# Performance work log

Hardware: AMD Instinct MI355X
Metric: run time of the kernel (lower is better)

## Reference

```python
import jax, jax.numpy as jnp
import numpy as np

N, E, IN, OUT, R, B = 20000, 640000, 128, 128, 65, 65
BN_EPS = 1e-5


def setup_inputs() -> dict:
    key = jax.random.key(0)
    ks = jax.random.split(key, 8)
    node_feats = jax.random.normal(ks[0], (N, IN), dtype=jnp.float32)
    src = jax.random.randint(ks[1], (E,), 0, N, dtype=jnp.int32)
    dst = jax.random.randint(ks[2], (E,), 0, N, dtype=jnp.int32)
    etype = jax.random.randint(ks[3], (E,), 0, R, dtype=jnp.int32)
    norm = jax.random.uniform(ks[4], (E, 1), dtype=jnp.float32)
    basis = jax.random.normal(ks[5], (B, IN, OUT), dtype=jnp.float32) * 0.05
    comp = jax.random.normal(ks[6], (R, B), dtype=jnp.float32) * 0.1
    h_bias = jnp.zeros((OUT,), dtype=jnp.float32)
    W_res = jax.random.normal(ks[7], (IN, OUT), dtype=jnp.float32) * 0.05
    b_res = jnp.zeros((OUT,), dtype=jnp.float32)
    gamma = jnp.ones((OUT,), dtype=jnp.float32)
    beta = jnp.zeros((OUT,), dtype=jnp.float32)
    return dict(node_feats=node_feats, src=src, dst=dst, etype=etype, norm=norm,
                basis=basis, comp=comp, h_bias=h_bias, W_res=W_res, b_res=b_res,
                gamma=gamma, beta=beta)


def reference(node_feats, src, dst, etype, norm, basis, comp, h_bias, W_res, b_res, gamma, beta):
    n, in_f = node_feats.shape
    r = comp.shape[0]
    # Basis decomposition: W_r = sum_b comp[r,b] * basis[b]  -> (R, in, out)
    W = jnp.einsum('rb,bio->rio', comp, basis)
    # Per-edge message x[src] * norm (norm is scalar per edge so it commutes
    # with the relation matmul). Aggregate per (dst, relation) first, then do
    # one dense relation-batched GEMM (mathematically identical to DGL's
    # per-edge transform + scatter-add, since everything is linear).
    msg = node_feats[src] * norm                       # (E, in)
    seg = dst.astype(jnp.int32) * r + etype            # combined (dst, rel) key
    S = jax.ops.segment_sum(msg, seg, num_segments=n * r).reshape(n, r, in_f)
    h = jnp.einsum('nri,rio->no', S, W) + h_bias       # (N, out)
    h = jax.nn.relu(h)                                 # conv activation (dropout p=0)
    # Residual branch: relu(Linear(x))
    h = h + jax.nn.relu(node_feats @ W_res + b_res)
    # BatchNorm1d (training mode: batch stats, biased variance)
    mean = jnp.mean(h, axis=0)
    var = jnp.var(h, axis=0)
    h = (h - mean) * jax.lax.rsqrt(var + BN_EPS) * gamma + beta
    return h
```

## Files before the change

### kernel.cpp

```cpp
#include <hip/hip_runtime.h>
#include <hip/hip_bf16.h>


#define N_NODES 20000
#define E_EDGES 640000
#define R_REL   65
#define TM      128
#define NB_RESID 313
#define MAX_TILES 5120
#define SCAT_CH 2560

typedef __attribute__((ext_vector_type(8))) short bf16x8;
typedef __attribute__((ext_vector_type(4))) float f32x4;
typedef __attribute__((ext_vector_type(4))) unsigned int u32x4;
typedef __attribute__((ext_vector_type(2))) unsigned int u32x2;

__device__ __forceinline__ unsigned short f2bf(float x) {
    union { float f; unsigned int u; } c; c.f = x;
    unsigned int b = c.u + 0x7fffu + ((c.u >> 16) & 1u);
    return (unsigned short)(b >> 16);
}
__device__ __forceinline__ float bf2f_lo(unsigned int u) {
    union { unsigned int u; float f; } c; c.u = u << 16; return c.f;
}
__device__ __forceinline__ float bf2f_hi(unsigned int u) {
    union { unsigned int u; float f; } c; c.u = u & 0xffff0000u; return c.f;
}
__device__ __forceinline__ void async16(const void* g, void* l) {
    __builtin_amdgcn_global_load_lds(
        (const __attribute__((address_space(1))) unsigned int*)g,
        (__attribute__((address_space(3))) unsigned int*)l, 16, 0, 0);
}
__device__ __forceinline__ int unperm(int p) {
    return (p & 64) + ((p & 3) << 4) + ((p >> 2) & 15);
}

__global__ void k_prep1(const float* __restrict__ comp, const float* __restrict__ basis,
                        float* __restrict__ W32, const int* __restrict__ et,
                        const int* __restrict__ dstA, int* __restrict__ ghist,
                        int* __restrict__ gh2, const float* __restrict__ node_feats,
                        unsigned short* __restrict__ node_bf) {
    __shared__ float lc[16 * 65];
    __shared__ int lh[R_REL];
    int b = blockIdx.x, t = threadIdx.x;
    if (b < 320) {
        int r0 = (b >> 6) * 16;
        int col = (b & 63) * 256 + t;
        for (int j = t; j < 16 * 65; j += 256) {
            int rr = r0 + j / 65;
            lc[j] = (rr < R_REL) ? comp[rr * 65 + (j % 65)] : 0.f;
        }
        __syncthreads();
        float acc[16];
#pragma unroll
        for (int j = 0; j < 16; ++j) acc[j] = 0.f;
        for (int k = 0; k < 65; ++k) {
            float v = basis[k * 16384 + col];
#pragma unroll
            for (int j = 0; j < 16; ++j) acc[j] += lc[j * 65 + k] * v;
        }
#pragma unroll
        for (int j = 0; j < 16; ++j) {
            int rr = r0 + j;
            if (rr < R_REL) W32[rr * 16384 + col] = acc[j];
        }
    } else if (b < 832) {
        if (t < R_REL) lh[t] = 0;
        __syncthreads();
        for (int i = (b - 320) * 256 + t; i < E_EDGES; i += 512 * 256) {
            atomicAdd(&lh[et[i]], 1);
            atomicAdd(&gh2[dstA[i]], 1);
        }
        __syncthreads();
        if (t < R_REL) atomicAdd(&ghist[t], lh[t]);
    } else {
        int i = (b - 832) * 256 + t;
        if (i < N_NODES * 32) {
            float4 v = reinterpret_cast<const float4*>(node_feats)[i];
            __hip_bfloat162 b0 = __float22bfloat162_rn(make_float2(v.x, v.y));
            __hip_bfloat162 b1 = __float22bfloat162_rn(make_float2(v.z, v.w));
            u32x2 pk;
            pk.x = *reinterpret_cast<unsigned int*>(&b0);
            pk.y = *reinterpret_cast<unsigned int*>(&b1);
            reinterpret_cast<u32x2*>(node_bf)[i] = pk;
        }
    }
}

__global__ void k_prep3(const int* __restrict__ gh2, int* __restrict__ cnt2,
                        int* __restrict__ seg, const int* __restrict__ ghist,
                        int* __restrict__ cnt, int* __restrict__ ntiles_p,
                        int* __restrict__ tile_rel, int* __restrict__ tile_start,
                        int* __restrict__ tile_len, const float* __restrict__ W32,
                        unsigned short* __restrict__ Wt, const float* __restrict__ Wresf,
                        unsigned short* __restrict__ Wrest) {
    int b = blockIdx.x, t = threadIdx.x;
    if (b < 80) {
        __shared__ int red[256];
        __shared__ int pref;
        int acc = 0;
        for (int i = t; i < b * 256; i += 256) acc += gh2[i];
        red[t] = acc;
        __syncthreads();
        for (int off = 128; off > 0; off >>= 1) {
            if (t < off) red[t] += red[t + off];
            __syncthreads();
        }
        if (t == 0) pref = red[0];
        __syncthreads();
        int i = b * 256 + t;
        int v = (i < N_NODES) ? gh2[i] : 0;
        red[t] = v;
        __syncthreads();
        for (int off = 1; off < 256; off <<= 1) {
            int x = (t >= off) ? red[t - off] : 0;
            __syncthreads();
            red[t] += x;
            __syncthreads();
        }
        int excl = red[t] - v + pref;
        if (i < N_NODES) {
            cnt2[i] = excl;
            seg[i] = excl;
            if (i == N_NODES - 1) seg[N_NODES] = excl + v;
        }
    } else if (b == 80) {
        __shared__ int base[R_REL + 1], tbase[R_REL + 1];
        int lane = t & 63;
        if (t < 64) {
            int v = ghist[lane];
            int x = v;
#pragma unroll
            for (int off = 1; off < 64; off <<= 1) {
                int y = __shfl_up(x, off);
                if (lane >= off) x += y;
            }
            base[lane] = x - v;
            if (lane == 63) {
                base[64] = x;
                base[65] = x + ghist[64];
            }
        }
        __syncthreads();
        if (t == 0) {
            int tb = 0;
            for (int r = 0; r < R_REL; ++r) {
                tbase[r] = tb;
                tb += (base[r + 1] - base[r] + TM - 1) / TM;
            }
            *ntiles_p = tb;
        }
        __syncthreads();
        if (t < R_REL) {
            cnt[t] = base[t];
            int s = base[t], e = base[t + 1], j = tbase[t];
            while (s < e) {
                int len = min(TM, e - s);
                tile_rel[j] = t; tile_start[j] = s; tile_len[j] = len;
                ++j; s += len;
            }
        }
    } else {
        __shared__ float tile[64][65];
        int bb = b - 81;
        const float* s; unsigned short* d; int sub;
        if (bb < R_REL * 4) { s = W32 + (size_t)(bb >> 2) * 16384; d = Wt + (size_t)(bb >> 2) * 16384; sub = bb & 3; }
        else { s = Wresf; d = Wrest; sub = bb - R_REL * 4; }
        int ot = (sub >> 1) & 1, itl = sub & 1;
        int tx = t & 63, ty = t >> 6;
        for (int it = 0; it < 16; ++it) {
            int i = ty + it * 4;
            tile[i][tx] = s[(itl * 64 + i) * 128 + ot * 64 + tx];
        }
        __syncthreads();
        for (int it = 0; it < 16; ++it) {
            int o = ty + it * 4;
            d[(ot * 64 + o) * 128 + itl * 64 + tx] = f2bf(tile[tx][o]);
        }
    }
}

__global__ void k_scatter2(const int* __restrict__ et, const int* __restrict__ srcA,
                           const int* __restrict__ dstA, const float* __restrict__ norm,
                           int* __restrict__ cnt, int* __restrict__ cnt2,
                           int* __restrict__ srcp, float* __restrict__ normp,
                           int* __restrict__ eidx) {
    __shared__ int lh[R_REL], lbase[R_REL];
    int c0 = blockIdx.x * SCAT_CH;
    int cend = min(c0 + SCAT_CH, E_EDGES);
    if (threadIdx.x < R_REL) lh[threadIdx.x] = 0;
    __syncthreads();
    for (int i = c0 + threadIdx.x; i < cend; i += 256) atomicAdd(&lh[et[i]], 1);
    __syncthreads();
    if (threadIdx.x < R_REL && lh[threadIdx.x] > 0)
        lbase[threadIdx.x] = atomicAdd(&cnt[threadIdx.x], lh[threadIdx.x]);
    __syncthreads();
    if (threadIdx.x < R_REL) lh[threadIdx.x] = 0;
    __syncthreads();
    for (int i = c0 + threadIdx.x; i < cend; i += 256) {
        int r = et[i];
        int p = lbase[r] + atomicAdd(&lh[r], 1);
        srcp[p] = srcA[i];
        normp[p] = norm[i];
        int pos = atomicAdd(&cnt2[dstA[i]], 1);
        eidx[pos] = p;
    }
}

__global__ __launch_bounds__(256, 2) void k_conv_gemm(
    const int* __restrict__ tile_rel, const int* __restrict__ tile_start,
    const int* __restrict__ tile_len, const int* __restrict__ ntiles_p,
    const int* __restrict__ srcp, const float* __restrict__ normp,
    const unsigned short* __restrict__ node_bf,
    const unsigned short* __restrict__ Wt, const unsigned short* __restrict__ Wrest,
    const float* __restrict__ b_res, unsigned short* __restrict__ t_out,
    float* __restrict__ resid) {
    __shared__ unsigned short Alds[128 * 128];
    __shared__ unsigned short Blds[128 * 128];
    __shared__ float snorm[128];
    int t = threadIdx.x;
    int w = t >> 6, lane = t & 63;
    int lrow = lane & 15, quad = lane >> 4;

    if (blockIdx.x < NB_RESID) {
        int wr = (w >> 1) * 32, wc = (w & 1) * 64;
        int row0 = blockIdx.x * 64;
        int nrows = min(64, N_NODES - row0);
#pragma unroll
        for (int it = 0; it < 8; ++it) {
            int j = t + 256 * it;
            int o = j >> 4, c = j & 15, cs = c ^ (o & 15);
            async16(Wrest + o * 128 + cs * 8, &Blds[o * 128 + c * 8]);
        }
#pragma unroll
        for (int it = 0; it < 4; ++it) {
            int j = t + 256 * it;
            int p = j >> 4, c = j & 15, cs = c ^ (p & 15);
            if (p < nrows)
                async16(node_bf + (size_t)(row0 + p) * 128 + cs * 8,
                        &Alds[p * 128 + c * 8]);
        }
        __syncthreads();
        f32x4 acc[2][4];
#pragma unroll
        for (int i = 0; i < 2; ++i)
#pragma unroll
            for (int j = 0; j < 4; ++j) acc[i][j] = (f32x4){0.f, 0.f, 0.f, 0.f};
#pragma unroll
        for (int ks = 0; ks < 4; ++ks) {
            int cs = (ks * 4 + quad) ^ lrow;
            bf16x8 af[2], bfr[4];
#pragma unroll
            for (int i = 0; i < 2; ++i)
                af[i] = *reinterpret_cast<const bf16x8*>(&Alds[(wr + i * 16 + lrow) * 128 + cs * 8]);
#pragma unroll
            for (int j = 0; j < 4; ++j)
                bfr[j] = *reinterpret_cast<const bf16x8*>(&Blds[(wc + j * 16 + lrow) * 128 + cs * 8]);
#pragma unroll
            for (int i = 0; i < 2; ++i)
#pragma unroll
                for (int j = 0; j < 4; ++j)
                    acc[i][j] = __builtin_amdgcn_mfma_f32_16x16x32_bf16(af[i], bfr[j], acc[i][j], 0, 0, 0);
        }
        float br0 = b_res[wc + lrow];
        float br1 = b_res[wc + 16 + lrow];
        float br2 = b_res[wc + 32 + lrow];
        float br3 = b_res[wc + 48 + lrow];
#pragma unroll
        for (int i = 0; i < 2; ++i) {
#pragma unroll
            for (int reg = 0; reg < 4; ++reg) {
                int grow = row0 + wr + i * 16 + quad * 4 + reg;
                if (grow < N_NODES) {
                    float4 v;
                    v.x = fmaxf(acc[i][0][reg] + br0, 0.f);
                    v.y = fmaxf(acc[i][1][reg] + br1, 0.f);
                    v.z = fmaxf(acc[i][2][reg] + br2, 0.f);
                    v.w = fmaxf(acc[i][3][reg] + br3, 0.f);
                    *reinterpret_cast<float4*>(resid + (size_t)grow * 128 + wc + lrow * 4) = v;
                }
            }
        }
        return;
    }

    int tid = blockIdx.x - NB_RESID;
    if (tid >= *ntiles_p) return;
    int r = tile_rel[tid], start = tile_start[tid], len = tile_len[tid];
    int wr = w * 32;
    const unsigned short* Wr = Wt + (size_t)r * 16384;
#pragma unroll
    for (int it = 0; it < 8; ++it) {
        int j = t + 256 * it;
        int o = j >> 4, c = j & 15, cs = c ^ (o & 15);
        async16(Wr + o * 128 + cs * 8, &Blds[o * 128 + c * 8]);
    }
#pragma unroll
    for (int it = 0; it < 8; ++it) {
        int j = t + 256 * it;
        int p = j >> 4, c = j & 15, cs = c ^ (p & 15);
        if (p < len)
            async16(node_bf + (size_t)srcp[start + p] * 128 + cs * 8,
                    &Alds[p * 128 + c * 8]);
    }
    if (t < TM && t < len) snorm[t] = normp[start + t];
    __syncthreads();

    f32x4 acc[2][8];
#pragma unroll
    for (int i = 0; i < 2; ++i)
#pragma unroll
        for (int j = 0; j < 8; ++j) acc[i][j] = (f32x4){0.f, 0.f, 0.f, 0.f};
#pragma unroll
    for (int ks = 0; ks < 4; ++ks) {
        int cs = (ks * 4 + quad) ^ lrow;
        bf16x8 af[2], bfr[8];
#pragma unroll
        for (int i = 0; i < 2; ++i)
            af[i] = *reinterpret_cast<const bf16x8*>(&Alds[(wr + i * 16 + lrow) * 128 + cs * 8]);
#pragma unroll
        for (int j = 0; j < 8; ++j)
            bfr[j] = *reinterpret_cast<const bf16x8*>(&Blds[(j * 16 + lrow) * 128 + cs * 8]);
#pragma unroll
        for (int i = 0; i < 2; ++i)
#pragma unroll
            for (int j = 0; j < 8; ++j)
                acc[i][j] = __builtin_amdgcn_mfma_f32_16x16x32_bf16(af[i], bfr[j], acc[i][j], 0, 0, 0);
    }

#pragma unroll
    for (int i = 0; i < 2; ++i) {
        int m0 = wr + i * 16 + quad * 4;
#pragma unroll
        for (int reg = 0; reg < 4; ++reg) {
            int m = m0 + reg;
            if (m < len) {
                float nm = snorm[m];
                float2 l0 = make_float2(acc[i][0][reg] * nm, acc[i][1][reg] * nm);
                float2 l1 = make_float2(acc[i][2][reg] * nm, acc[i][3][reg] * nm);
                float2 h0 = make_float2(acc[i][4][reg] * nm, acc[i][5][reg] * nm);
                float2 h1 = make_float2(acc[i][6][reg] * nm, acc[i][7][reg] * nm);
                __hip_bfloat162 bl0 = __float22bfloat162_rn(l0);
                __hip_bfloat162 bl1 = __float22bfloat162_rn(l1);
                __hip_bfloat162 bh0 = __float22bfloat162_rn(h0);
                __hip_bfloat162 bh1 = __float22bfloat162_rn(h1);
                u32x2 s0, s1;
                s0.x = *reinterpret_cast<unsigned int*>(&bl0);
                s0.y = *reinterpret_cast<unsigned int*>(&bl1);
                s1.x = *reinterpret_cast<unsigned int*>(&bh0);
                s1.y = *reinterpret_cast<unsigned int*>(&bh1);
                unsigned short* rowp = t_out + (size_t)(start + m) * 128;
                *reinterpret_cast<u32x2*>(rowp + lrow * 4)      = s0;
                *reinterpret_cast<u32x2*>(rowp + 64 + lrow * 4) = s1;
            }
        }
    }
}

__global__ __launch_bounds__(256) void k_reduce_fused(
    const unsigned short* __restrict__ t, const int* __restrict__ seg,
    const int* __restrict__ eidx, const float* __restrict__ resid,
    const float* __restrict__ h_bias, float* __restrict__ h,
    float* __restrict__ colsum, float* __restrict__ colsumsq) {
    __shared__ float cs1[128], cs2[128], sbias[128];
    if (threadIdx.x < 128) {
        cs1[threadIdx.x] = 0.f; cs2[threadIdx.x] = 0.f;
        sbias[threadIdx.x] = h_bias[unperm(threadIdx.x)];
    }
    __syncthreads();
    int w = threadIdx.x >> 6, lane = threadIdx.x & 63;
    int g = lane >> 4, c = lane & 15;
    for (int k = 0; k < 2; ++k) {
        int d = blockIdx.x * 8 + k * 4 + w;
        int a = seg[d], b = seg[d + 1];
        float s[8];
#pragma unroll
        for (int kk = 0; kk < 8; ++kk) s[kk] = 0.f;
        for (int q = a + g; q < b; q += 32) {
            int er[8];
#pragma unroll
            for (int kk = 0; kk < 8; ++kk) {
                int row = q + 4 * kk;
                er[kk] = eidx[(row < b) ? row : a];
            }
            u32x4 v[8];
#pragma unroll
            for (int kk = 0; kk < 8; ++kk) {
                v[kk] = *reinterpret_cast<const u32x4*>(t + (size_t)er[kk] * 128 + c * 8);
                if (q + 4 * kk >= b) v[kk] = (u32x4){0u, 0u, 0u, 0u};
            }
#pragma unroll
            for (int kk = 0; kk < 8; ++kk)
#pragma unroll
                for (int j = 0; j < 4; ++j) {
                    s[2 * j]     += bf2f_lo(v[kk][j]);
                    s[2 * j + 1] += bf2f_hi(v[kk][j]);
                }
        }
#pragma unroll
        for (int kk = 0; kk < 8; ++kk) {
            s[kk] += __shfl_xor(s[kk], 16);
            s[kk] += __shfl_xor(s[kk], 32);
        }
        if (g == 0) {
            const float* rp = resid + (size_t)d * 128 + c * 8;
            float4 r0 = *reinterpret_cast<const float4*>(rp);
            float4 r1 = *reinterpret_cast<const float4*>(rp + 4);
            float rr[8] = {r0.x, r0.y, r0.z, r0.w, r1.x, r1.y, r1.z, r1.w};
            float v[8];
#pragma unroll
            for (int kk = 0; kk < 8; ++kk)
                v[kk] = fmaxf(s[kk] + sbias[c * 8 + kk], 0.f) + rr[kk];
            float* hp = h + (size_t)d * 128 + c * 8;
            *reinterpret_cast<float4*>(hp)     = make_float4(v[0], v[1], v[2], v[3]);
            *reinterpret_cast<float4*>(hp + 4) = make_float4(v[4], v[5], v[6], v[7]);
#pragma unroll
            for (int kk = 0; kk < 8; ++kk) {
                atomicAdd(&cs1[c * 8 + kk], v[kk]);
                atomicAdd(&cs2[c * 8 + kk], v[kk] * v[kk]);
            }
        }
    }
    __syncthreads();
    if (threadIdx.x < 128) {
        atomicAdd(&colsum[threadIdx.x], cs1[threadIdx.x]);
        atomicAdd(&colsumsq[threadIdx.x], cs2[threadIdx.x]);
    }
}

__global__ void k_bn(float* __restrict__ h, const float* __restrict__ colsum,
                     const float* __restrict__ colsumsq, const float* __restrict__ gamma,
                     const float* __restrict__ beta) {
    __shared__ float sc[128], sh[128], tile[8][128];
    int t = threadIdx.x;
    if (t < 128) {
        int n = unperm(t);
        float m = colsum[t] * (1.f / N_NODES);
        float var = colsumsq[t] * (1.f / N_NODES) - m * m;
        float s = gamma[n] * rsqrtf(var + 1e-5f);
        sc[t] = s;
        sh[t] = beta[n] - m * s;
    }
    __syncthreads();
    int r = t >> 5;
    int p0 = (t & 31) * 4;
    int n0 = (p0 & 64) + ((p0 >> 2) & 15);
    for (int row0 = blockIdx.x * 8; row0 < N_NODES; row0 += gridDim.x * 8) {
        int row = row0 + r;
        float4 v = make_float4(0.f, 0.f, 0.f, 0.f);
        if (row < N_NODES) v = *reinterpret_cast<float4*>(h + (size_t)row * 128 + p0);
        v.x = v.x * sc[p0] + sh[p0];
        v.y = v.y * sc[p0 + 1] + sh[p0 + 1];
        v.z = v.z * sc[p0 + 2] + sh[p0 + 2];
        v.w = v.w * sc[p0 + 3] + sh[p0 + 3];
        tile[r][n0]      = v.x;
        tile[r][n0 + 16] = v.y;
        tile[r][n0 + 32] = v.z;
        tile[r][n0 + 48] = v.w;
        __syncthreads();
        if (row < N_NODES)
            *reinterpret_cast<float4*>(h + (size_t)row * 128 + p0) =
                *reinterpret_cast<float4*>(&tile[r][p0]);
        __syncthreads();
    }
}

extern "C" void kernel_launch(void* const* d_in, const int* in_sizes, int n_in,
                              void* d_out, int out_size, void* d_ws, size_t ws_size,
                              hipStream_t stream) {
    (void)in_sizes; (void)n_in; (void)out_size; (void)ws_size;
    const float* node_feats = (const float*)d_in[0];
    const int* src    = (const int*)d_in[1];
    const int* dst    = (const int*)d_in[2];
    const int* etype  = (const int*)d_in[3];
    const float* norm = (const float*)d_in[4];
    const float* basis = (const float*)d_in[5];
    const float* comp  = (const float*)d_in[6];
    const float* h_bias = (const float*)d_in[7];
    const float* W_res  = (const float*)d_in[8];
    const float* b_res  = (const float*)d_in[9];
    const float* gamma  = (const float*)d_in[10];
    const float* beta   = (const float*)d_in[11];

    char* ws = (char*)d_ws;
    int* ghist      = (int*)(ws + 0);
    int* cnt        = (int*)(ws + 1024);
    int* ntiles_p   = (int*)(ws + 2048);
    float* colsum   = (float*)(ws + 2560);
    float* colsumsq = (float*)(ws + 3072);
    int* gh2        = (int*)(ws + 8192);
    int* tile_rel   = (int*)(ws + 88192);
    int* tile_start = (int*)(ws + 129152);
    int* tile_len   = (int*)(ws + 170112);
    unsigned short* Wt      = (unsigned short*)(ws + 211072);
    unsigned short* Wrest   = (unsigned short*)(ws + 2340992);
    unsigned short* node_bf = (unsigned short*)(ws + 2373760);
    int* srcp       = (int*)(ws + 7493760);
    float* normp    = (float*)(ws + 10053760);
    int* eidx       = (int*)(ws + 12613760);
    float* resid    = (float*)(ws + 15173760);
    int* seg        = (int*)(ws + 25413760);
    int* cnt2       = (int*)(ws + 25493776);
    const long T_BASE = 25573776L;
    float* W32      = (float*)(ws + T_BASE);
    unsigned short* t_buf = (unsigned short*)(ws + T_BASE);
    float* hacc = (float*)d_out;

    hipMemsetAsync(ws, 0, 88192, stream);
    k_prep1<<<3332, 256, 0, stream>>>(comp, basis, W32, etype, dst, ghist, gh2,
                                      node_feats, node_bf);
    k_prep3<<<345, 256, 0, stream>>>(gh2, cnt2, seg, ghist, cnt, ntiles_p,
                                     tile_rel, tile_start, tile_len,
                                     W32, Wt, W_res, Wrest);
    k_scatter2<<<(E_EDGES + SCAT_CH - 1) / SCAT_CH, 256, 0, stream>>>(
        etype, src, dst, norm, cnt, cnt2, srcp, normp, eidx);
    k_conv_gemm<<<NB_RESID + MAX_TILES, 256, 0, stream>>>(
        tile_rel, tile_start, tile_len, ntiles_p, srcp, normp, node_bf,
        Wt, Wrest, b_res, t_buf, resid);
    k_reduce_fused<<<N_NODES / 8, 256, 0, stream>>>(t_buf, seg, eidx, resid,
                                                    h_bias, hacc, colsum, colsumsq);
    k_bn<<<2500, 256, 0, stream>>>(hacc, colsum, colsumsq, gamma, beta);
}
```

Baseline: 344.5 us.

## Bucket edges by (dst group, relation) so transformed rows gather locally

Edges are now sorted by a combined key of destination group (dst>>7) and relation instead of by relation alone, using a per-key histogram, scan and direct atomic scatter. Tiles are built per key with a smaller TM of 64, and the GEMM kernel uses a 64-row A tile with launch bounds raised to allow more blocks per CU. The intent is that the per-edge transformed rows read by the reduce kernel sit close together in memory, improving cache locality of the gather, and that occupancy rises. The cost is many more, smaller, partially filled tiles, each of which reloads a full 128x128 weight block. Edge order inside a bucket now depends on atomic ordering, and the reduce kernel processes 32 nodes per block.

```diff
diff --git a/kernel.cpp b/kernel.cpp
--- a/kernel.cpp
+++ b/kernel.cpp
@@ -5,10 +5,11 @@
 #define N_NODES 20000
 #define E_EDGES 640000
 #define R_REL   65
-#define TM      128
+#define NGRP_B  157
+#define NKEY_B  (NGRP_B * R_REL)
 #define NB_RESID 313
-#define MAX_TILES 5120
-#define SCAT_CH 2560
+#define MAX_TILES 20480
+#define TM      64
 
 typedef __attribute__((ext_vector_type(8))) short bf16x8;
 typedef __attribute__((ext_vector_type(4))) float f32x4;
@@ -37,11 +38,10 @@
 
 __global__ void k_prep1(const float* __restrict__ comp, const float* __restrict__ basis,
                         float* __restrict__ W32, const int* __restrict__ et,
-                        const int* __restrict__ dstA, int* __restrict__ ghist,
+                        const int* __restrict__ dstA, int* __restrict__ gh3,
                         int* __restrict__ gh2, const float* __restrict__ node_feats,
                         unsigned short* __restrict__ node_bf) {
     __shared__ float lc[16 * 65];
-    __shared__ int lh[R_REL];
     int b = blockIdx.x, t = threadIdx.x;
     if (b < 320) {
         int r0 = (b >> 6) * 16;
@@ -65,14 +65,11 @@
             if (rr < R_REL) W32[rr * 16384 + col] = acc[j];
         }
     } else if (b < 832) {
-        if (t < R_REL) lh[t] = 0;
-        __syncthreads();
         for (int i = (b - 320) * 256 + t; i < E_EDGES; i += 512 * 256) {
-            atomicAdd(&lh[et[i]], 1);
-            atomicAdd(&gh2[dstA[i]], 1);
-        }
-        __syncthreads();
-        if (t < R_REL) atomicAdd(&ghist[t], lh[t]);
+            int d = dstA[i];
+            atomicAdd(&gh3[(d >> 7) * 65 + et[i]], 1);
+            atomicAdd(&gh2[d], 1);
+        }
     } else {
         int i = (b - 832) * 256 + t;
         if (i < N_NODES * 32) {
@@ -87,19 +84,17 @@
     }
 }
 
-__global__ void k_prep3(const int* __restrict__ gh2, int* __restrict__ cnt2,
-                        int* __restrict__ seg, const int* __restrict__ ghist,
-                        int* __restrict__ cnt, int* __restrict__ ntiles_p,
-                        int* __restrict__ tile_rel, int* __restrict__ tile_start,
-                        int* __restrict__ tile_len, const float* __restrict__ W32,
-                        unsigned short* __restrict__ Wt, const float* __restrict__ Wresf,
-                        unsigned short* __restrict__ Wrest) {
+__global__ void k_prep3(const int* __restrict__ gh3, int* __restrict__ segB,
+                        int* __restrict__ cnt3, const int* __restrict__ gh2,
+                        int* __restrict__ cnt2, int* __restrict__ seg,
+                        const float* __restrict__ W32, unsigned short* __restrict__ Wt,
+                        const float* __restrict__ Wresf, unsigned short* __restrict__ Wrest) {
     int b = blockIdx.x, t = threadIdx.x;
-    if (b < 80) {
+    if (b < 40) {
         __shared__ int red[256];
         __shared__ int pref;
         int acc = 0;
-        for (int i = t; i < b * 256; i += 256) acc += gh2[i];
+        for (int i = t; i < b * 256; i += 256) acc += gh3[i];
         red[t] = acc;
         __syncthreads();
         for (int off = 128; off > 0; off >>= 1) {
@@ -109,7 +104,7 @@
         if (t == 0) pref = red[0];
         __syncthreads();
         int i = b * 256 + t;
-        int v = (i < N_NODES) ? gh2[i] : 0;
+        int v = (i < NKEY_B) ? gh3[i] : 0;
         red[t] = v;
         __syncthreads();
         for (int off = 1; off < 256; off <<= 1) {
@@ -119,50 +114,44 @@
             __syncthreads();
         }
         int excl = red[t] - v + pref;
+        if (i < NKEY_B) {
+            segB[i] = excl;
+            cnt3[i] = excl;
+            if (i == NKEY_B - 1) segB[NKEY_B] = excl + v;
+        }
+    } else if (b < 120) {
+        __shared__ int red[256];
+        __shared__ int pref;
+        int b2 = b - 40;
+        int acc = 0;
+        for (int i = t; i < b2 * 256; i += 256) acc += gh2[i];
+        red[t] = acc;
+        __syncthreads();
+        for (int off = 128; off > 0; off >>= 1) {
+            if (t < off) red[t] += red[t + off];
+            __syncthreads();
+        }
+        if (t == 0) pref = red[0];
+        __syncthreads();
+        int i = b2 * 256 + t;
+        int v = (i < N_NODES) ? gh2[i] : 0;
+        red[t] = v;
+        __syncthreads();
+        for (int off = 1; off < 256; off <<= 1) {
+            int x = (t >= off) ? red[t - off] : 0;
+            __syncthreads();
+            red[t] += x;
+            __syncthreads();
+        }
+        int excl = red[t] - v + pref;
         if (i < N_NODES) {
             cnt2[i] = excl;
             seg[i] = excl;
             if (i == N_NODES - 1) seg[N_NODES] = excl + v;
         }
-    } else if (b == 80) {
-        __shared__ int base[R_REL + 1], tbase[R_REL + 1];
-        int lane = t & 63;
-        if (t < 64) {
-            int v = ghist[lane];
-            int x = v;
-#pragma unroll
-            for (int off = 1; off < 64; off <<= 1) {
-                int y = __shfl_up(x, off);
-                if (lane >= off) x += y;
-            }
-            base[lane] = x - v;
-            if (lane == 63) {
-                base[64] = x;
-                base[65] = x + ghist[64];
-            }
-        }
-        __syncthreads();
-        if (t == 0) {
-            int tb = 0;
-            for (int r = 0; r < R_REL; ++r) {
-                tbase[r] = tb;
-                tb += (base[r + 1] - base[r] + TM - 1) / TM;
-            }
-            *ntiles_p = tb;
-        }
-        __syncthreads();
-        if (t < R_REL) {
-            cnt[t] = base[t];
-            int s = base[t], e = base[t + 1], j = tbase[t];
-            while (s < e) {
-                int len = min(TM, e - s);
-                tile_rel[j] = t; tile_start[j] = s; tile_len[j] = len;
-                ++j; s += len;
-            }
-        }
     } else {
         __shared__ float tile[64][65];
-        int bb = b - 81;
+        int bb = b - 120;
         const float* s; unsigned short* d; int sub;
         if (bb < R_REL * 4) { s = W32 + (size_t)(bb >> 2) * 16384; d = Wt + (size_t)(bb >> 2) * 16384; sub = bb & 3; }
         else { s = Wresf; d = Wrest; sub = bb - R_REL * 4; }
@@ -182,42 +171,51 @@
 
 __global__ void k_scatter2(const int* __restrict__ et, const int* __restrict__ srcA,
                            const int* __restrict__ dstA, const float* __restrict__ norm,
-                           int* __restrict__ cnt, int* __restrict__ cnt2,
+                           int* __restrict__ cnt3, int* __restrict__ cnt2,
                            int* __restrict__ srcp, float* __restrict__ normp,
-                           int* __restrict__ eidx) {
-    __shared__ int lh[R_REL], lbase[R_REL];
-    int c0 = blockIdx.x * SCAT_CH;
-    int cend = min(c0 + SCAT_CH, E_EDGES);
-    if (threadIdx.x < R_REL) lh[threadIdx.x] = 0;
-    __syncthreads();
-    for (int i = c0 + threadIdx.x; i < cend; i += 256) atomicAdd(&lh[et[i]], 1);
-    __syncthreads();
-    if (threadIdx.x < R_REL && lh[threadIdx.x] > 0)
-        lbase[threadIdx.x] = atomicAdd(&cnt[threadIdx.x], lh[threadIdx.x]);
-    __syncthreads();
-    if (threadIdx.x < R_REL) lh[threadIdx.x] = 0;
-    __syncthreads();
-    for (int i = c0 + threadIdx.x; i < cend; i += 256) {
-        int r = et[i];
-        int p = lbase[r] + atomicAdd(&lh[r], 1);
+                           int* __restrict__ eidx, const int* __restrict__ segB,
+                           int* __restrict__ ntiles_p, int* __restrict__ tile_r,
+                           int* __restrict__ tile_start, int* __restrict__ tile_len) {
+    int b = blockIdx.x, t = threadIdx.x;
+    if (b < 2500) {
+        int i = b * 256 + t;
+        if (i >= E_EDGES) return;
+        int d = dstA[i];
+        int key = (d >> 7) * 65 + et[i];
+        int p = atomicAdd(&cnt3[key], 1);
         srcp[p] = srcA[i];
         normp[p] = norm[i];
-        int pos = atomicAdd(&cnt2[dstA[i]], 1);
+        int pos = atomicAdd(&cnt2[d], 1);
         eidx[pos] = p;
-    }
-}
-
-__global__ __launch_bounds__(256, 2) void k_conv_gemm(
-    const int* __restrict__ tile_rel, const int* __restrict__ tile_start,
+    } else {
+        int i = (b - 2500) * 256 + t;
+        if (i < NKEY_B) {
+            int s = segB[i], e = segB[i + 1];
+            int len = e - s;
+            if (len > 0) {
+                int nt = (len + TM - 1) / TM;
+                int base = atomicAdd(ntiles_p, nt);
+                for (int k = 0; k < nt; ++k) {
+                    tile_r[base + k] = i % 65;
+                    tile_start[base + k] = s + k * TM;
+                    tile_len[base + k] = min(TM, len - k * TM);
+                }
+            }
+        }
+    }
+}
+
+__global__ __launch_bounds__(256, 3) void k_conv_gemm(
+    const int* __restrict__ tile_r, const int* __restrict__ tile_start,
     const int* __restrict__ tile_len, const int* __restrict__ ntiles_p,
     const int* __restrict__ srcp, const float* __restrict__ normp,
     const unsigned short* __restrict__ node_bf,
     const unsigned short* __restrict__ Wt, const unsigned short* __restrict__ Wrest,
     const float* __restrict__ b_res, unsigned short* __restrict__ t_out,
     float* __restrict__ resid) {
-    __shared__ unsigned short Alds[128 * 128];
     __shared__ unsigned short Blds[128 * 128];
-    __shared__ float snorm[128];
+    __shared__ unsigned short Alds[64 * 128];
+    __shared__ float snorm[64];
     int t = threadIdx.x;
     int w = t >> 6, lane = t & 63;
     int lrow = lane & 15, quad = lane >> 4;
@@ -286,8 +284,7 @@
 
     int tid = blockIdx.x - NB_RESID;
     if (tid >= *ntiles_p) return;
-    int r = tile_rel[tid], start = tile_start[tid], len = tile_len[tid];
-    int wr = w * 32;
+    int r = tile_r[tid], start = tile_start[tid], len = tile_len[tid];
     const unsigned short* Wr = Wt + (size_t)r * 16384;
 #pragma unroll
     for (int it = 0; it < 8; ++it) {
@@ -296,7 +293,7 @@
         async16(Wr + o * 128 + cs * 8, &Blds[o * 128 + c * 8]);
     }
 #pragma unroll
-    for (int it = 0; it < 8; ++it) {
+    for (int it = 0; it < 4; ++it) {
         int j = t + 256 * it;
         int p = j >> 4, c = j & 15, cs = c ^ (p & 15);
         if (p < len)
@@ -306,53 +303,43 @@
     if (t < TM && t < len) snorm[t] = normp[start + t];
     __syncthreads();
 
-    f32x4 acc[2][8];
-#pragma unroll
-    for (int i = 0; i < 2; ++i)
-#pragma unroll
-        for (int j = 0; j < 8; ++j) acc[i][j] = (f32x4){0.f, 0.f, 0.f, 0.f};
+    int wr = w * 16;
+    if (wr >= len) return;
+    f32x4 acc[8];
+#pragma unroll
+    for (int j = 0; j < 8; ++j) acc[j] = (f32x4){0.f, 0.f, 0.f, 0.f};
 #pragma unroll
     for (int ks = 0; ks < 4; ++ks) {
         int cs = (ks * 4 + quad) ^ lrow;
-        bf16x8 af[2], bfr[8];
-#pragma unroll
-        for (int i = 0; i < 2; ++i)
-            af[i] = *reinterpret_cast<const bf16x8*>(&Alds[(wr + i * 16 + lrow) * 128 + cs * 8]);
-#pragma unroll
-        for (int j = 0; j < 8; ++j)
-            bfr[j] = *reinterpret_cast<const bf16x8*>(&Blds[(j * 16 + lrow) * 128 + cs * 8]);
-#pragma unroll
-        for (int i = 0; i < 2; ++i)
-#pragma unroll
-            for (int j = 0; j < 8; ++j)
-                acc[i][j] = __builtin_amdgcn_mfma_f32_16x16x32_bf16(af[i], bfr[j], acc[i][j], 0, 0, 0);
-    }
-
-#pragma unroll
-    for (int i = 0; i < 2; ++i) {
-        int m0 = wr + i * 16 + quad * 4;
-#pragma unroll
-        for (int reg = 0; reg < 4; ++reg) {
-            int m = m0 + reg;
-            if (m < len) {
-                float nm = snorm[m];
-                float2 l0 = make_float2(acc[i][0][reg] * nm, acc[i][1][reg] * nm);
-                float2 l1 = make_float2(acc[i][2][reg] * nm, acc[i][3][reg] * nm);
-                float2 h0 = make_float2(acc[i][4][reg] * nm, acc[i][5][reg] * nm);
-                float2 h1 = make_float2(acc[i][6][reg] * nm, acc[i][7][reg] * nm);
-                __hip_bfloat162 bl0 = __float22bfloat162_rn(l0);
-                __hip_bfloat162 bl1 = __float22bfloat162_rn(l1);
-                __hip_bfloat162 bh0 = __float22bfloat162_rn(h0);
-                __hip_bfloat162 bh1 = __float22bfloat162_rn(h1);
-                u32x2 s0, s1;
-                s0.x = *reinterpret_cast<unsigned int*>(&bl0);
-                s0.y = *reinterpret_cast<unsigned int*>(&bl1);
-                s1.x = *reinterpret_cast<unsigned int*>(&bh0);
-                s1.y = *reinterpret_cast<unsigned int*>(&bh1);
-                unsigned short* rowp = t_out + (size_t)(start + m) * 128;
-                *reinterpret_cast<u32x2*>(rowp + lrow * 4)      = s0;
-                *reinterpret_cast<u32x2*>(rowp + 64 + lrow * 4) = s1;
-            }
+        bf16x8 af = *reinterpret_cast<const bf16x8*>(&Alds[(wr + lrow) * 128 + cs * 8]);
+#pragma unroll
+        for (int j = 0; j < 8; ++j) {
+            bf16x8 bfr = *reinterpret_cast<const bf16x8*>(&Blds[(j * 16 + lrow) * 128 + cs * 8]);
+            acc[j] = __builtin_amdgcn_mfma_f32_16x16x32_bf16(af, bfr, acc[j], 0, 0, 0);
+        }
+    }
+
+#pragma unroll
+    for (int reg = 0; reg < 4; ++reg) {
+        int m = wr + quad * 4 + reg;
+        if (m < len) {
+            float nm = snorm[m];
+            float2 l0 = make_float2(acc[0][reg] * nm, acc[1][reg] * nm);
+            float2 l1 = make_float2(acc[2][reg] * nm, acc[3][reg] * nm);
+            float2 h0 = make_float2(acc[4][reg] * nm, acc[5][reg] * nm);
+            float2 h1 = make_float2(acc[6][reg] * nm, acc[7][reg] * nm);
+            __hip_bfloat162 bl0 = __float22bfloat162_rn(l0);
+            __hip_bfloat162 bl1 = __float22bfloat162_rn(l1);
+            __hip_bfloat162 bh0 = __float22bfloat162_rn(h0);
+            __hip_bfloat162 bh1 = __float22bfloat162_rn(h1);
+            u32x2 s0, s1;
+            s0.x = *reinterpret_cast<unsigned int*>(&bl0);
+            s0.y = *reinterpret_cast<unsigned int*>(&bl1);
+            s1.x = *reinterpret_cast<unsigned int*>(&bh0);
+            s1.y = *reinterpret_cast<unsigned int*>(&bh1);
+            unsigned short* rowp = t_out + (size_t)(start + m) * 128;
+            *reinterpret_cast<u32x2*>(rowp + lrow * 4)      = s0;
+            *reinterpret_cast<u32x2*>(rowp + 64 + lrow * 4) = s1;
         }
     }
 }
@@ -370,8 +357,9 @@
     __syncthreads();
     int w = threadIdx.x >> 6, lane = threadIdx.x & 63;
     int g = lane >> 4, c = lane & 15;
-    for (int k = 0; k < 2; ++k) {
-        int d = blockIdx.x * 8 + k * 4 + w;
+    for (int k = 0; k < 8; ++k) {
+        int d = blockIdx.x * 32 + k * 4 + w;
+        if (d >= N_NODES) continue;
         int a = seg[d], b = seg[d + 1];
         float s[8];
 #pragma unroll
@@ -483,41 +471,42 @@
     const float* beta   = (const float*)d_in[11];
 
     char* ws = (char*)d_ws;
-    int* ghist      = (int*)(ws + 0);
-    int* cnt        = (int*)(ws + 1024);
-    int* ntiles_p   = (int*)(ws + 2048);
-    float* colsum   = (float*)(ws + 2560);
-    float* colsumsq = (float*)(ws + 3072);
-    int* gh2        = (int*)(ws + 8192);
-    int* tile_rel   = (int*)(ws + 88192);
-    int* tile_start = (int*)(ws + 129152);
-    int* tile_len   = (int*)(ws + 170112);
-    unsigned short* Wt      = (unsigned short*)(ws + 211072);
-    unsigned short* Wrest   = (unsigned short*)(ws + 2340992);
-    unsigned short* node_bf = (unsigned short*)(ws + 2373760);
-    int* srcp       = (int*)(ws + 7493760);
-    float* normp    = (float*)(ws + 10053760);
-    int* eidx       = (int*)(ws + 12613760);
-    float* resid    = (float*)(ws + 15173760);
-    int* seg        = (int*)(ws + 25413760);
-    int* cnt2       = (int*)(ws + 25493776);
-    const long T_BASE = 25573776L;
+    float* colsum   = (float*)(ws + 0);
+    float* colsumsq = (float*)(ws + 512);
+    int* ntiles_p   = (int*)(ws + 1024);
+    int* gh3        = (int*)(ws + 1088);
+    int* gh2        = (int*)(ws + 41920);
+    int* segB       = (int*)(ws + 121920);
+    int* cnt3       = (int*)(ws + 162752);
+    int* seg        = (int*)(ws + 203584);
+    int* cnt2       = (int*)(ws + 283648);
+    int* tile_r     = (int*)(ws + 363648);
+    int* tile_start = (int*)(ws + 445568);
+    int* tile_len   = (int*)(ws + 527488);
+    unsigned short* Wt      = (unsigned short*)(ws + 609408);
+    unsigned short* Wrest   = (unsigned short*)(ws + 2739328);
+    unsigned short* node_bf = (unsigned short*)(ws + 2772096);
+    int* srcp       = (int*)(ws + 7892096);
+    float* normp    = (float*)(ws + 10452096);
+    int* eidx       = (int*)(ws + 13012096);
+    float* resid    = (float*)(ws + 15572096);
+    const long T_BASE = 25812096L;
     float* W32      = (float*)(ws + T_BASE);
     unsigned short* t_buf = (unsigned short*)(ws + T_BASE);
     float* hacc = (float*)d_out;
 
-    hipMemsetAsync(ws, 0, 88192, stream);
-    k_prep1<<<3332, 256, 0, stream>>>(comp, basis, W32, etype, dst, ghist, gh2,
+    hipMemsetAsync(ws, 0, 121920, stream);
+    k_prep1<<<3332, 256, 0, stream>>>(comp, basis, W32, etype, dst, gh3, gh2,
                                       node_feats, node_bf);
-    k_prep3<<<345, 256, 0, stream>>>(gh2, cnt2, seg, ghist, cnt, ntiles_p,
-                                     tile_rel, tile_start, tile_len,
+    k_prep3<<<384, 256, 0, stream>>>(gh3, segB, cnt3, gh2, cnt2, seg,
                                      W32, Wt, W_res, Wrest);
-    k_scatter2<<<(E_EDGES + SCAT_CH - 1) / SCAT_CH, 256, 0, stream>>>(
-        etype, src, dst, norm, cnt, cnt2, srcp, normp, eidx);
+    k_scatter2<<<2540, 256, 0, stream>>>(etype, src, dst, norm, cnt3, cnt2,
+                                         srcp, normp, eidx, segB, ntiles_p,
+                                         tile_r, tile_start, tile_len);
     k_conv_gemm<<<NB_RESID + MAX_TILES, 256, 0, stream>>>(
-        tile_rel, tile_start, tile_len, ntiles_p, srcp, normp, node_bf,
+        tile_r, tile_start, tile_len, ntiles_p, srcp, normp, node_bf,
         Wt, Wrest, b_res, t_buf, resid);
-    k_reduce_fused<<<N_NODES / 8, 256, 0, stream>>>(t_buf, seg, eidx, resid,
-                                                    h_bias, hacc, colsum, colsumsq);
+    k_reduce_fused<<<626, 256, 0, stream>>>(t_buf, seg, eidx, resid,
+                                            h_bias, hacc, colsum, colsumsq);
     k_bn<<<2500, 256, 0, stream>>>(hacc, colsum, colsumsq, gamma, beta);
 }
```

New measurement: 409.4 us. 18.8% more time.
